# Kernel optimization log

Measured on AMD Instinct MI355X. Metric: run time of the kernel, lower is better.

Reference implementation:

```python
import jax, jax.numpy as jnp
import numpy as np

B, NHID, L = 8, 256, 2048
NHEAD, HEAD_DIM = 8, 64
D = NHEAD * HEAD_DIM          # 512, q/k/v channels
DO = NHEAD * NHID             # 2048, output channels of WO
WIN = 3                       # unfold_size


def setup_inputs() -> dict:
    key = jax.random.key(0)
    ks = jax.random.split(key, 5)
    s = 0.02
    return {
        "x": jax.random.normal(ks[0], (B, NHID, L, 1), dtype=jnp.float32),
        "Wq": jax.random.normal(ks[1], (NHID, D), dtype=jnp.float32) * s,
        "bq": jnp.zeros((D,), jnp.float32),
        "Wk": jax.random.normal(ks[2], (NHID, D), dtype=jnp.float32) * s,
        "bk": jnp.zeros((D,), jnp.float32),
        "Wv": jax.random.normal(ks[3], (NHID, D), dtype=jnp.float32) * s,
        "bv": jnp.zeros((D,), jnp.float32),
        "Wo": jax.random.normal(ks[4], (D, DO), dtype=jnp.float32) * s,
        "bo": jnp.zeros((DO,), jnp.float32),
    }


def reference(x, Wq, bq, Wk, bk, Wv, bv, Wo, bo):
    # x: [B, nhid, L, 1]. 1x1 Conv2D over channel dim == dense on last axis.
    b, nhid, l, _ = x.shape
    xt = x[..., 0].transpose(0, 2, 1)            # [B, L, nhid]
    q = xt @ Wq + bq                             # [B, L, D]
    k = xt @ Wk + bk
    v = xt @ Wv + bv

    def windows(t):
        # SAME-padded sliding window of size 3 over L (tf.image.extract_patches)
        tp = jnp.pad(t, ((0, 0), (1, 1), (0, 0)))
        return jnp.stack([tp[:, i:i + l] for i in range(WIN)], axis=2)  # [B, L, 3, D]

    # D splits as (nhead, head_dim) with nhead outer, matching the reshapes
    # [B, nhead, head_dim, ...] in the original.
    qr = q.reshape(b, l, NHEAD, HEAD_DIM)                  # [B, L, n, h]
    kw = windows(k).reshape(b, l, WIN, NHEAD, HEAD_DIM)    # [B, L, w, n, h]
    vw = windows(v).reshape(b, l, WIN, NHEAD, HEAD_DIM)

    scale = jnp.asarray(1.0 / np.sqrt(HEAD_DIM), x.dtype)
    scores = jnp.einsum('blnh,blwnh->blnw', qr, kw) * scale  # [B, L, n, w]
    alphas = jax.nn.softmax(scores, axis=-1)                 # softmax over window
    att = jnp.einsum('blnw,blwnh->blnh', alphas, vw)         # [B, L, n, h]
    att = att.reshape(b, l, NHEAD * HEAD_DIM)                # [B, L, D]

    out = att @ Wo + bo                                      # [B, L, nhead*nhid]
    return out.transpose(0, 2, 1)[..., None]                 # [B, nhead*nhid, L, 1]
```

## Files before the change

kernel.cpp:

```cpp
#include <hip/hip_runtime.h>
#include <cstdint>
#include <cmath>

#define B_    8
#define NHID_ 256
#define L_    2048
#define D_    512
#define DO_   2048
#define QKVN  1536

using u16    = unsigned short;
using short8 = __attribute__((ext_vector_type(8))) short;
using f32x4  = __attribute__((ext_vector_type(4))) float;

typedef __attribute__((address_space(1))) void gv_t;
typedef __attribute__((address_space(3))) void lv_t;

__device__ inline void llds16(const void* g, void* l) {
  __builtin_amdgcn_global_load_lds((const gv_t*)g, (lv_t*)l, 16, 0, 0);
}

__device__ inline u16 f32_to_bf16(float f) {
  unsigned u = __float_as_uint(f);
  u += 0x7fffu + ((u >> 16) & 1u);
  return (u16)(u >> 16);
}

__device__ inline void load8(const u16* p, float f[8]) {
  uint4 u = *reinterpret_cast<const uint4*>(p);
  f[0] = __uint_as_float(u.x << 16); f[1] = __uint_as_float(u.x & 0xffff0000u);
  f[2] = __uint_as_float(u.y << 16); f[3] = __uint_as_float(u.y & 0xffff0000u);
  f[4] = __uint_as_float(u.z << 16); f[5] = __uint_as_float(u.z & 0xffff0000u);
  f[6] = __uint_as_float(u.w << 16); f[7] = __uint_as_float(u.w & 0xffff0000u);
}

template <int R, int C>
__device__ inline void t64(const float* __restrict__ src, u16* __restrict__ dst,
                           int id, float (*tile)[65]) {
  constexpr int TPR = C / 64;
  constexpr int PER = (R / 64) * TPR;
  int z = id / PER, rem = id % PER;
  int ry = rem / TPR, cx = rem % TPR;
  src += (size_t)z * R * C;
  dst += (size_t)z * R * C;
  int c0 = cx * 64, r0 = ry * 64;
  int tx = threadIdx.x, ty = threadIdx.y;
#pragma unroll
  for (int i = 0; i < 8; ++i)
    tile[ty + i * 8][tx] = src[(size_t)(r0 + ty + i * 8) * C + c0 + tx];
  __syncthreads();
#pragma unroll
  for (int i = 0; i < 8; ++i)
    dst[(size_t)(c0 + ty + i * 8) * R + r0 + tx] = f32_to_bf16(tile[tx][ty + i * 8]);
}

#define PREP_WQ   1024
#define PREP_WK   1056
#define PREP_WV   1088
#define PREP_WO   1120
#define PREP_BIAS 1376
#define PREP_NB   1379

__global__ void prep_all(const float* __restrict__ x,
                         const float* __restrict__ Wq, const float* __restrict__ Wk,
                         const float* __restrict__ Wv, const float* __restrict__ Wo,
                         const float* __restrict__ bq, const float* __restrict__ bk,
                         const float* __restrict__ bv,
                         u16* __restrict__ xb, u16* __restrict__ wqkvT,
                         u16* __restrict__ woT, float* __restrict__ bqkv) {
  __shared__ float tile[64][65];
  int bid = blockIdx.x;
  if (bid < PREP_WQ) {
    t64<NHID_, L_>(x, xb, bid, tile);
  } else if (bid < PREP_WK) {
    t64<NHID_, D_>(Wq, wqkvT, bid - PREP_WQ, tile);
  } else if (bid < PREP_WV) {
    t64<NHID_, D_>(Wk, wqkvT + 512 * NHID_, bid - PREP_WK, tile);
  } else if (bid < PREP_WO) {
    t64<NHID_, D_>(Wv, wqkvT + 1024 * NHID_, bid - PREP_WV, tile);
  } else if (bid < PREP_BIAS) {
    t64<D_, DO_>(Wo, woT, bid - PREP_WO, tile);
  } else {
    int d = (bid - PREP_BIAS) * 512 + threadIdx.y * 64 + threadIdx.x;
    float v = (d < 512) ? bq[d] : (d < 1024 ? bk[d - 512] : bv[d - 1024]);
    bqkv[d] = v;
  }
}

#define BM 128
#define BN 128
#define BK 64

template <int K>
__device__ inline void gemm_tile(const u16* __restrict__ gA, const u16* __restrict__ gB,
                                 int m0, int n0, u16* As, u16* Bs, f32x4 (&acc)[4][4]) {
  const int tid = threadIdx.x;
  const int wave = tid >> 6, lane = tid & 63;
  const int wm = wave >> 1, wn = wave & 1;
  const int r8 = lane >> 3;
  const int kc = ((lane & 7) ^ r8) * 8;
  const int fr = lane & 15;
  const int fx = fr & 7;
  const int kq = lane >> 4;

  auto stage = [&](int k0) {
#pragma unroll
    for (int t = 0; t < 4; ++t) {
      int chunk = wave * 4 + t;
      int row = chunk * 8 + r8;
      llds16(gA + (size_t)(m0 + row) * K + k0 + kc, (char*)As + chunk * 1024);
      llds16(gB + (size_t)(n0 + row) * K + k0 + kc, (char*)Bs + chunk * 1024);
    }
  };

  stage(0);
#pragma unroll
  for (int i = 0; i < 4; ++i)
#pragma unroll
    for (int j = 0; j < 4; ++j) acc[i][j] = f32x4{0.f, 0.f, 0.f, 0.f};

  for (int k0 = 0;;) {
    __syncthreads();
#pragma unroll
    for (int ks = 0; ks < 2; ++ks) {
      short8 a[4], b[4];
      const int slot = (((ks * 4 + kq) ^ fx)) * 8;
#pragma unroll
      for (int mt = 0; mt < 4; ++mt)
        a[mt] = *(const short8*)(As + (wm * 64 + mt * 16 + fr) * BK + slot);
#pragma unroll
      for (int nt = 0; nt < 4; ++nt)
        b[nt] = *(const short8*)(Bs + (wn * 64 + nt * 16 + fr) * BK + slot);
#pragma unroll
      for (int mt = 0; mt < 4; ++mt)
#pragma unroll
        for (int nt = 0; nt < 4; ++nt)
          acc[mt][nt] = __builtin_amdgcn_mfma_f32_16x16x32_bf16(a[mt], b[nt], acc[mt][nt], 0, 0, 0);
    }
    k0 += BK;
    if (k0 >= K) break;
    __syncthreads();
    stage(k0);
  }
}

__global__ __launch_bounds__(256) void qkv_gemm(const u16* __restrict__ xb,
                                                const u16* __restrict__ wT,
                                                const float* __restrict__ bqkv,
                                                u16* __restrict__ qkv) {
  __shared__ __align__(16) u16 As[BM * BK];
  __shared__ __align__(16) u16 Bs[BN * BK];
  int id = blockIdx.x;
  int swz = (id & 7) * 192 + (id >> 3);
  int n0 = (swz % 12) * BN;
  int m0 = (swz / 12) * BM;
  f32x4 acc[4][4];
  gemm_tile<NHID_>(xb, wT, m0, n0, As, Bs, acc);
  const int lane = threadIdx.x & 63, wave = threadIdx.x >> 6;
  const int wm = wave >> 1, wn = wave & 1;
#pragma unroll
  for (int mt = 0; mt < 4; ++mt) {
    int row0 = m0 + wm * 64 + mt * 16 + (lane >> 4) * 4;
#pragma unroll
    for (int nt = 0; nt < 4; ++nt) {
      int col = n0 + wn * 64 + nt * 16 + (lane & 15);
      float bias = bqkv[col];
#pragma unroll
      for (int r = 0; r < 4; ++r)
        qkv[(size_t)(row0 + r) * QKVN + col] = f32_to_bf16(acc[mt][nt][r] + bias);
    }
  }
}

__global__ __launch_bounds__(256) void out_gemm(const u16* __restrict__ woT,
                                                const u16* __restrict__ att,
                                                const float* __restrict__ bo,
                                                float* __restrict__ out) {
  __shared__ __align__(16) u16 As[BM * BK];
  __shared__ __align__(16) u16 Bs[BN * BK];
  int id = blockIdx.x;
  int swz = (id & 7) * 256 + (id >> 3);
  int b = swz >> 8;
  int rem = swz & 255;
  int m0 = (rem >> 4) * BM;
  int n0 = (rem & 15) * BN;
  const u16* gB = att + (size_t)b * L_ * D_;
  f32x4 acc[4][4];
  gemm_tile<D_>(woT, gB, m0, n0, As, Bs, acc);
  const int lane = threadIdx.x & 63, wave = threadIdx.x >> 6;
  const int wm = wave >> 1, wn = wave & 1;
  float* outb = out + (size_t)b * DO_ * L_;
#pragma unroll
  for (int mt = 0; mt < 4; ++mt) {
    int row0 = m0 + wm * 64 + mt * 16 + (lane >> 4) * 4;
#pragma unroll
    for (int r = 0; r < 4; ++r) {
      float bias = bo[row0 + r];
#pragma unroll
      for (int nt = 0; nt < 4; ++nt) {
        int col = n0 + wn * 64 + nt * 16 + (lane & 15);
        outb[(size_t)(row0 + r) * L_ + col] = acc[mt][nt][r] + bias;
      }
    }
  }
}

__global__ __launch_bounds__(512) void attn_kernel(const u16* __restrict__ qkv,
                                                   u16* __restrict__ att) {
  const int wave = threadIdx.x >> 6, lane = threadIdx.x & 63;
  int id = blockIdx.x;
  int swz = (id & 7) * 128 + (id >> 3);
  const int g = swz * 8 + wave;
  const int gr0 = g * 2;
  const int l0 = gr0 & (L_ - 1);
  const int c0 = (lane >> 3) * 64 + (lane & 7) * 8;

  float q[2][8];
  load8(qkv + (size_t)gr0 * QKVN + c0, q[0]);
  load8(qkv + (size_t)(gr0 + 1) * QKVN + c0, q[1]);

  float kk[4][8], vv[4][8];
#pragma unroll
  for (int j = 0; j < 4; ++j) {
    bool valid = !(j == 0 && l0 == 0) && !(j == 3 && l0 == L_ - 2);
    if (valid) {
      const u16* base = qkv + (size_t)(gr0 - 1 + j) * QKVN;
      load8(base + 512 + c0, kk[j]);
      load8(base + 1024 + c0, vv[j]);
    } else {
#pragma unroll
      for (int t = 0; t < 8; ++t) { kk[j][t] = 0.f; vv[j][t] = 0.f; }
    }
  }

  float s[2][3];
#pragma unroll
  for (int r = 0; r < 2; ++r)
#pragma unroll
    for (int w = 0; w < 3; ++w) {
      float a = 0.f;
#pragma unroll
      for (int t = 0; t < 8; ++t) a = fmaf(q[r][t], kk[r + w][t], a);
      s[r][w] = a;
    }
#pragma unroll
  for (int off = 1; off < 8; off <<= 1) {
#pragma unroll
    for (int r = 0; r < 2; ++r) {
      s[r][0] += __shfl_xor(s[r][0], off);
      s[r][1] += __shfl_xor(s[r][1], off);
      s[r][2] += __shfl_xor(s[r][2], off);
    }
  }

#pragma unroll
  for (int r = 0; r < 2; ++r) {
    float s0 = s[r][0] * 0.125f, s1 = s[r][1] * 0.125f, s2 = s[r][2] * 0.125f;
    float mx = fmaxf(s0, fmaxf(s1, s2));
    float e0 = __expf(s0 - mx), e1 = __expf(s1 - mx), e2 = __expf(s2 - mx);
    float inv = 1.f / (e0 + e1 + e2);
    float a0 = e0 * inv, a1 = e1 * inv, a2 = e2 * inv;

    u16 o16[8];
#pragma unroll
    for (int t = 0; t < 8; ++t) {
      float o = a0 * vv[r][t] + a1 * vv[r + 1][t] + a2 * vv[r + 2][t];
      o16[t] = f32_to_bf16(o);
    }
    uint4 pk;
    pk.x = (unsigned)o16[0] | ((unsigned)o16[1] << 16);
    pk.y = (unsigned)o16[2] | ((unsigned)o16[3] << 16);
    pk.z = (unsigned)o16[4] | ((unsigned)o16[5] << 16);
    pk.w = (unsigned)o16[6] | ((unsigned)o16[7] << 16);
    *reinterpret_cast<uint4*>(att + (size_t)(gr0 + r) * D_ + c0) = pk;
  }
}

extern "C" void kernel_launch(void* const* d_in, const int* in_sizes, int n_in,
                              void* d_out, int out_size, void* d_ws, size_t ws_size,
                              hipStream_t stream) {
  const float* x  = (const float*)d_in[0];
  const float* Wq = (const float*)d_in[1];
  const float* bq = (const float*)d_in[2];
  const float* Wk = (const float*)d_in[3];
  const float* bk = (const float*)d_in[4];
  const float* Wv = (const float*)d_in[5];
  const float* bv = (const float*)d_in[6];
  const float* Wo = (const float*)d_in[7];
  const float* bo = (const float*)d_in[8];
  float* out = (float*)d_out;

  char* ws = (char*)d_ws;
  u16*   xb    = (u16*)(ws + 0);
  u16*   wqkvT = (u16*)(ws + 8388608);
  u16*   woT   = (u16*)(ws + 9175040);
  float* bqkv  = (float*)(ws + 11272192);
  u16*   qkv   = (u16*)(ws + 11278336);
  u16*   att   = (u16*)(ws + 61609984);

  prep_all<<<PREP_NB, dim3(64, 8), 0, stream>>>(x, Wq, Wk, Wv, Wo, bq, bk, bv,
                                                xb, wqkvT, woT, bqkv);

  qkv_gemm<<<(QKVN / BN) * ((B_ * L_) / BM), 256, 0, stream>>>(xb, wqkvT, bqkv, qkv);

  attn_kernel<<<(B_ * L_) / 16, 512, 0, stream>>>(qkv, att);

  out_gemm<<<(L_ / BN) * (DO_ / BM) * B_, 256, 0, stream>>>(woT, att, bo, out);
}
```

Before: 217.1 us.

## Process two M-tiles per GEMM block, prefetching the next tile's first K-slice

Both GEMMs now have each workgroup compute two consecutive 128-row output tiles, halving the grid size. While the current tile finishes its last K step, the first K-slice of the next tile is already being loaded, and the epilogue is passed in as a lambda. The goal is to amortise launch and prologue cost and hide the first-stage load latency of the second tile. The cost is fewer workgroups on the GPU, and the stores of the first tile are serialised before the second tile's compute.

```diff
diff --git a/kernel.cpp b/kernel.cpp
--- a/kernel.cpp
+++ b/kernel.cpp
@@ -91,9 +91,9 @@
 #define BN 128
 #define BK 64
 
-template <int K>
-__device__ inline void gemm_tile(const u16* __restrict__ gA, const u16* __restrict__ gB,
-                                 int m0, int n0, u16* As, u16* Bs, f32x4 (&acc)[4][4]) {
+template <int K, int T, typename F>
+__device__ inline void gemm_multi(const u16* __restrict__ gA, const u16* __restrict__ gB,
+                                  int m0_base, int n0, u16* As, u16* Bs, F&& writeC) {
   const int tid = threadIdx.x;
   const int wave = tid >> 6, lane = tid & 63;
   const int wm = wave >> 1, wn = wave & 1;
@@ -103,7 +103,7 @@
   const int fx = fr & 7;
   const int kq = lane >> 4;
 
-  auto stage = [&](int k0) {
+  auto stage = [&](int m0, int k0) {
 #pragma unroll
     for (int t = 0; t < 4; ++t) {
       int chunk = wave * 4 + t;
@@ -113,34 +113,40 @@
     }
   };
 
-  stage(0);
-#pragma unroll
-  for (int i = 0; i < 4; ++i)
-#pragma unroll
-    for (int j = 0; j < 4; ++j) acc[i][j] = f32x4{0.f, 0.f, 0.f, 0.f};
-
-  for (int k0 = 0;;) {
-    __syncthreads();
-#pragma unroll
-    for (int ks = 0; ks < 2; ++ks) {
-      short8 a[4], b[4];
-      const int slot = (((ks * 4 + kq) ^ fx)) * 8;
-#pragma unroll
-      for (int mt = 0; mt < 4; ++mt)
-        a[mt] = *(const short8*)(As + (wm * 64 + mt * 16 + fr) * BK + slot);
-#pragma unroll
-      for (int nt = 0; nt < 4; ++nt)
-        b[nt] = *(const short8*)(Bs + (wn * 64 + nt * 16 + fr) * BK + slot);
-#pragma unroll
-      for (int mt = 0; mt < 4; ++mt)
+  stage(m0_base, 0);
+  f32x4 acc[4][4];
+
+  for (int t = 0; t < T; ++t) {
+    const int m0 = m0_base + t * BM;
+#pragma unroll
+    for (int i = 0; i < 4; ++i)
+#pragma unroll
+      for (int j = 0; j < 4; ++j) acc[i][j] = f32x4{0.f, 0.f, 0.f, 0.f};
+
+    for (int k0 = 0; k0 < K; k0 += BK) {
+      __syncthreads();
+#pragma unroll
+      for (int ks = 0; ks < 2; ++ks) {
+        short8 a[4], b[4];
+        const int slot = (((ks * 4 + kq) ^ fx)) * 8;
+#pragma unroll
+        for (int mt = 0; mt < 4; ++mt)
+          a[mt] = *(const short8*)(As + (wm * 64 + mt * 16 + fr) * BK + slot);
 #pragma unroll
         for (int nt = 0; nt < 4; ++nt)
-          acc[mt][nt] = __builtin_amdgcn_mfma_f32_16x16x32_bf16(a[mt], b[nt], acc[mt][nt], 0, 0, 0);
-    }
-    k0 += BK;
-    if (k0 >= K) break;
-    __syncthreads();
-    stage(k0);
+          b[nt] = *(const short8*)(Bs + (wn * 64 + nt * 16 + fr) * BK + slot);
+#pragma unroll
+        for (int mt = 0; mt < 4; ++mt)
+#pragma unroll
+          for (int nt = 0; nt < 4; ++nt)
+            acc[mt][nt] = __builtin_amdgcn_mfma_f32_16x16x32_bf16(a[mt], b[nt], acc[mt][nt], 0, 0, 0);
+      }
+      __syncthreads();
+      int nk = k0 + BK;
+      if (nk < K) stage(m0, nk);
+      else if (t + 1 < T) stage(m0 + BM, 0);
+    }
+    writeC(m0, acc);
   }
 }
 
@@ -151,25 +157,26 @@
   __shared__ __align__(16) u16 As[BM * BK];
   __shared__ __align__(16) u16 Bs[BN * BK];
   int id = blockIdx.x;
-  int swz = (id & 7) * 192 + (id >> 3);
+  int swz = (id & 7) * 96 + (id >> 3);
   int n0 = (swz % 12) * BN;
-  int m0 = (swz / 12) * BM;
-  f32x4 acc[4][4];
-  gemm_tile<NHID_>(xb, wT, m0, n0, As, Bs, acc);
-  const int lane = threadIdx.x & 63, wave = threadIdx.x >> 6;
-  const int wm = wave >> 1, wn = wave & 1;
-#pragma unroll
-  for (int mt = 0; mt < 4; ++mt) {
-    int row0 = m0 + wm * 64 + mt * 16 + (lane >> 4) * 4;
-#pragma unroll
-    for (int nt = 0; nt < 4; ++nt) {
-      int col = n0 + wn * 64 + nt * 16 + (lane & 15);
-      float bias = bqkv[col];
-#pragma unroll
-      for (int r = 0; r < 4; ++r)
-        qkv[(size_t)(row0 + r) * QKVN + col] = f32_to_bf16(acc[mt][nt][r] + bias);
-    }
-  }
+  int m0_base = (swz / 12) * (2 * BM);
+  gemm_multi<NHID_, 2>(xb, wT, m0_base, n0, As, Bs,
+    [&](int m0, f32x4 (&acc)[4][4]) {
+      const int lane = threadIdx.x & 63, wave = threadIdx.x >> 6;
+      const int wm = wave >> 1, wn = wave & 1;
+#pragma unroll
+      for (int mt = 0; mt < 4; ++mt) {
+        int row0 = m0 + wm * 64 + mt * 16 + (lane >> 4) * 4;
+#pragma unroll
+        for (int nt = 0; nt < 4; ++nt) {
+          int col = n0 + wn * 64 + nt * 16 + (lane & 15);
+          float bias = bqkv[col];
+#pragma unroll
+          for (int r = 0; r < 4; ++r)
+            qkv[(size_t)(row0 + r) * QKVN + col] = f32_to_bf16(acc[mt][nt][r] + bias);
+        }
+      }
+    });
 }
 
 __global__ __launch_bounds__(256) void out_gemm(const u16* __restrict__ woT,
@@ -179,30 +186,31 @@
   __shared__ __align__(16) u16 As[BM * BK];
   __shared__ __align__(16) u16 Bs[BN * BK];
   int id = blockIdx.x;
-  int swz = (id & 7) * 256 + (id >> 3);
-  int b = swz >> 8;
-  int rem = swz & 255;
-  int m0 = (rem >> 4) * BM;
+  int swz = (id & 7) * 128 + (id >> 3);
+  int b = swz >> 7;
+  int rem = swz & 127;
   int n0 = (rem & 15) * BN;
+  int m0_base = (rem >> 4) * (2 * BM);
   const u16* gB = att + (size_t)b * L_ * D_;
-  f32x4 acc[4][4];
-  gemm_tile<D_>(woT, gB, m0, n0, As, Bs, acc);
-  const int lane = threadIdx.x & 63, wave = threadIdx.x >> 6;
-  const int wm = wave >> 1, wn = wave & 1;
   float* outb = out + (size_t)b * DO_ * L_;
-#pragma unroll
-  for (int mt = 0; mt < 4; ++mt) {
-    int row0 = m0 + wm * 64 + mt * 16 + (lane >> 4) * 4;
-#pragma unroll
-    for (int r = 0; r < 4; ++r) {
-      float bias = bo[row0 + r];
-#pragma unroll
-      for (int nt = 0; nt < 4; ++nt) {
-        int col = n0 + wn * 64 + nt * 16 + (lane & 15);
-        outb[(size_t)(row0 + r) * L_ + col] = acc[mt][nt][r] + bias;
+  gemm_multi<D_, 2>(woT, gB, m0_base, n0, As, Bs,
+    [&](int m0, f32x4 (&acc)[4][4]) {
+      const int lane = threadIdx.x & 63, wave = threadIdx.x >> 6;
+      const int wm = wave >> 1, wn = wave & 1;
+#pragma unroll
+      for (int mt = 0; mt < 4; ++mt) {
+        int row0 = m0 + wm * 64 + mt * 16 + (lane >> 4) * 4;
+#pragma unroll
+        for (int r = 0; r < 4; ++r) {
+          float bias = bo[row0 + r];
+#pragma unroll
+          for (int nt = 0; nt < 4; ++nt) {
+            int col = n0 + wn * 64 + nt * 16 + (lane & 15);
+            outb[(size_t)(row0 + r) * L_ + col] = acc[mt][nt][r] + bias;
+          }
+        }
       }
-    }
-  }
+    });
 }
 
 __global__ __launch_bounds__(512) void attn_kernel(const u16* __restrict__ qkv,
@@ -301,9 +309,9 @@
   prep_all<<<PREP_NB, dim3(64, 8), 0, stream>>>(x, Wq, Wk, Wv, Wo, bq, bk, bv,
                                                 xb, wqkvT, woT, bqkv);
 
-  qkv_gemm<<<(QKVN / BN) * ((B_ * L_) / BM), 256, 0, stream>>>(xb, wqkvT, bqkv, qkv);
+  qkv_gemm<<<768, 256, 0, stream>>>(xb, wqkvT, bqkv, qkv);
 
   attn_kernel<<<(B_ * L_) / 16, 512, 0, stream>>>(qkv, att);
 
-  out_gemm<<<(L_ / BN) * (DO_ / BM) * B_, 256, 0, stream>>>(woT, att, bo, out);
-}
+  out_gemm<<<1024, 256, 0, stream>>>(woT, att, bo, out);
+}
```

After: 223.3 us. +2.8%, slower.
